# Performance work log

Measured on AMD Instinct MI355X. Metric: run time of the kernel, lower is better.

Reference implementation:

```python
import jax, jax.numpy as jnp
import numpy as np

NUM_HEADS = 16


def setup_inputs() -> dict:
    key = jax.random.key(0)
    k1, k2, k3 = jax.random.split(key, 3)
    B, S, E = 2, 2048, 1024
    hidden_states = jax.random.normal(k1, (B, S, E), dtype=jnp.float32)
    c_attn_w = jax.random.normal(k2, (E, 3 * E), dtype=jnp.float32) * 0.02
    c_attn_b = jnp.zeros((3 * E,), dtype=jnp.float32)
    c_proj_w = jax.random.normal(k3, (E, E), dtype=jnp.float32) * 0.02
    c_proj_b = jnp.zeros((E,), dtype=jnp.float32)
    return {
        "hidden_states": hidden_states,
        "c_attn_w": c_attn_w,
        "c_attn_b": c_attn_b,
        "c_proj_w": c_proj_w,
        "c_proj_b": c_proj_b,
    }


def reference(hidden_states, c_attn_w, c_attn_b, c_proj_w, c_proj_b):
    B, S, E = hidden_states.shape
    H = NUM_HEADS
    D = E // H
    # Conv1D: qkv projection -> [B, S, 3E]
    qkv = jnp.einsum("bse,ef->bsf", hidden_states, c_attn_w) + c_attn_b
    q, k, v = jnp.split(qkv, 3, axis=-1)
    # split heads -> [B, H, S, D]
    def heads(x):
        return x.reshape(B, S, H, D).transpose(0, 2, 1, 3)
    q, k, v = heads(q), heads(k), heads(v)
    # scaled QK^T -> [B, H, S, S]
    scale = jnp.asarray(D, dtype=q.dtype) ** 0.5
    attn_weights = jnp.einsum("bhqd,bhkd->bhqk", q, k) / scale
    # causal mask (bias buffer): True on/below diagonal
    causal = jnp.tril(jnp.ones((S, S), dtype=bool))
    mask_value = jnp.finfo(attn_weights.dtype).min
    attn_weights = jnp.where(causal[None, None, :, :], attn_weights, mask_value)
    attn_weights = jax.nn.softmax(attn_weights, axis=-1)
    # attn @ V -> merge heads -> [B, S, E]
    attn_out = jnp.einsum("bhqk,bhkd->bhqd", attn_weights, v)
    attn_out = attn_out.transpose(0, 2, 1, 3).reshape(B, S, E)
    # output projection (Conv1D)
    out = jnp.einsum("bse,ef->bsf", attn_out, c_proj_w) + c_proj_b
    return out
```

## Files before the change

kernel.cpp:

```cpp
#include <hip/hip_runtime.h>
#include <stdint.h>

typedef __attribute__((ext_vector_type(8))) __bf16 bf16x8;
typedef __attribute__((ext_vector_type(4))) __bf16 bf16x4;
typedef __attribute__((ext_vector_type(4))) float f32x4;

#define MFMA16(a, b, c) __builtin_amdgcn_mfma_f32_16x16x32_bf16(a, b, c, 0, 0, 0)

__device__ __forceinline__ void async_ld16(const __bf16* g, __bf16* lds_base) {
    __builtin_amdgcn_global_load_lds(
        (const __attribute__((address_space(1))) void*)g,
        (__attribute__((address_space(3))) void*)lds_base, 16, 0, 0);
}

__global__ __launch_bounds__(256) void k_prep(
    const float* __restrict__ hs, const float* __restrict__ w1,
    const float* __restrict__ w2, __bf16* __restrict__ hsb,
    __bf16* __restrict__ w1t, __bf16* __restrict__ w2t) {
    __shared__ __bf16 tile[32][33];
    int bid = blockIdx.x, tid = threadIdx.x;
    if (bid < 4096) {
        int i = (bid * 256 + tid) * 4;
        float4 v = *(const float4*)(hs + i);
        bf16x4 o;
        o.x = (__bf16)v.x; o.y = (__bf16)v.y; o.z = (__bf16)v.z; o.w = (__bf16)v.w;
        *(bf16x4*)(hsb + i) = o;
        return;
    }
    const float* in; __bf16* out; int C, tb;
    if (bid < 7168) { in = w1; out = w1t; C = 3072; tb = bid - 4096; }
    else            { in = w2; out = w2t; C = 1024; tb = bid - 7168; }
    const int R = 1024;
    int ntc = C >> 5;
    int c0 = (tb % ntc) * 32, r0 = (tb / ntc) * 32;
    int tx = tid & 31, ty = tid >> 5;
#pragma unroll
    for (int i = 0; i < 4; i++)
        tile[ty + i * 8][tx] = (__bf16)in[(size_t)(r0 + ty + i * 8) * C + c0 + tx];
    __syncthreads();
#pragma unroll
    for (int i = 0; i < 4; i++)
        out[(size_t)(c0 + ty + i * 8) * R + r0 + tx] = tile[tx][ty + i * 8];
}

__global__ __launch_bounds__(256, 2) void k_gemm_qkv(
    const __bf16* __restrict__ A, const __bf16* __restrict__ Bt,
    const float* __restrict__ bias,
    __bf16* __restrict__ Qo, __bf16* __restrict__ Ko, __bf16* __restrict__ Vo) {
    __shared__ __bf16 As[128 * 32];
    __shared__ __bf16 Bs[128 * 32];
    const int Kd = 1024;
    int n0 = blockIdx.x * 128, m0 = blockIdx.y * 128;
    int tid = threadIdx.x;
    int wv = tid >> 6, lane = tid & 63;
    int wm = (wv >> 1) * 64, wn = (wv & 1) * 64;
    int quad = lane >> 4, l16 = lane & 15;
    int lrow = lane >> 2, lcol = (lane & 3) * 8;
    f32x4 acc[4][4] = {};
    for (int k0 = 0; k0 < Kd; k0 += 32) {
        __syncthreads();
#pragma unroll
        for (int r = 0; r < 2; r++) {
            int row = r * 64 + wv * 16;
            async_ld16(&A[(size_t)(m0 + row + lrow) * Kd + k0 + lcol], &As[row * 32]);
            async_ld16(&Bt[(size_t)(n0 + row + lrow) * Kd + k0 + lcol], &Bs[row * 32]);
        }
        __syncthreads();
        bf16x8 af[4], bfr[4];
#pragma unroll
        for (int i = 0; i < 4; i++)
            af[i] = *(const bf16x8*)(&As[(wm + i * 16 + l16) * 32 + quad * 8]);
#pragma unroll
        for (int j = 0; j < 4; j++)
            bfr[j] = *(const bf16x8*)(&Bs[(wn + j * 16 + l16) * 32 + quad * 8]);
#pragma unroll
        for (int i = 0; i < 4; i++)
#pragma unroll
            for (int j = 0; j < 4; j++)
                acc[i][j] = MFMA16(af[i], bfr[j], acc[i][j]);
    }
#pragma unroll
    for (int i = 0; i < 4; i++) {
#pragma unroll
        for (int j = 0; j < 4; j++) {
            int n = n0 + wn + j * 16 + l16;
            float bv = bias[n];
            int sec = n >> 10, nl = n & 1023;
            int h = nl >> 6, d = nl & 63;
            int mbase = m0 + wm + i * 16 + quad * 4;
            int bb = mbase >> 11, s = mbase & 2047;
            if (sec == 2) {
                bf16x4 v4;
#pragma unroll
                for (int r = 0; r < 4; r++) v4[r] = (__bf16)(acc[i][j][r] + bv);
                *(bf16x4*)(&Vo[((size_t)(bb * 16 + h) * 64 + d) * 2048 + s]) = v4;
            } else {
                __bf16* dst = sec == 0 ? Qo : Ko;
                float scl = (sec == 0) ? 0.1803368801f : 1.0f;
#pragma unroll
                for (int r = 0; r < 4; r++)
                    dst[((size_t)(bb * 16 + h) * 2048 + (s + r)) * 64 + d] =
                        (__bf16)((acc[i][j][r] + bv) * scl);
            }
        }
    }
}

__global__ __launch_bounds__(256, 2) void k_gemm_proj(
    const __bf16* __restrict__ A, const __bf16* __restrict__ Bt,
    const float* __restrict__ bias, float* __restrict__ out) {
    __shared__ __bf16 As[64 * 32];
    __shared__ __bf16 Bs[128 * 32];
    const int Kd = 1024;
    int n0 = blockIdx.x * 128, m0 = blockIdx.y * 64;
    int tid = threadIdx.x;
    int wv = tid >> 6, lane = tid & 63;
    int wm = (wv >> 1) * 32, wn = (wv & 1) * 64;
    int quad = lane >> 4, l16 = lane & 15;
    int lrow = lane >> 2, lcol = (lane & 3) * 8;
    f32x4 acc[2][4] = {};
    for (int k0 = 0; k0 < Kd; k0 += 32) {
        __syncthreads();
        async_ld16(&A[(size_t)(m0 + wv * 16 + lrow) * Kd + k0 + lcol], &As[(wv * 16) * 32]);
#pragma unroll
        for (int r = 0; r < 2; r++) {
            int row = r * 64 + wv * 16;
            async_ld16(&Bt[(size_t)(n0 + row + lrow) * Kd + k0 + lcol], &Bs[row * 32]);
        }
        __syncthreads();
        bf16x8 af[2], bfr[4];
#pragma unroll
        for (int i = 0; i < 2; i++)
            af[i] = *(const bf16x8*)(&As[(wm + i * 16 + l16) * 32 + quad * 8]);
#pragma unroll
        for (int j = 0; j < 4; j++)
            bfr[j] = *(const bf16x8*)(&Bs[(wn + j * 16 + l16) * 32 + quad * 8]);
#pragma unroll
        for (int i = 0; i < 2; i++)
#pragma unroll
            for (int j = 0; j < 4; j++)
                acc[i][j] = MFMA16(af[i], bfr[j], acc[i][j]);
    }
#pragma unroll
    for (int i = 0; i < 2; i++) {
#pragma unroll
        for (int j = 0; j < 4; j++) {
            int n = n0 + wn + j * 16 + l16;
            float bv = bias[n];
#pragma unroll
            for (int r = 0; r < 4; r++) {
                int m = m0 + wm + i * 16 + quad * 4 + r;
                out[(size_t)m * 1024 + n] = acc[i][j][r] + bv;
            }
        }
    }
}

__device__ const int ATT_ORDER[24] = {7, 8, 10, 12, 14, 16, 18, 20, 22, 23, 6, 21,
                                      5, 19, 4, 17, 3, 15, 2, 13, 1, 11, 0, 9};

__global__ __launch_bounds__(256, 4) void k_attn(
    const __bf16* __restrict__ Qg, const __bf16* __restrict__ Kg,
    const __bf16* __restrict__ Vtg, __bf16* __restrict__ Op, float* __restrict__ Lp) {
    __shared__ __bf16 Ks[64 * 72];
    __shared__ __bf16 Vt[64 * 72];
    __shared__ __bf16 Ps[128 * 72];
    int bh = blockIdx.x & 31;
    int slot = ATT_ORDER[blockIdx.x >> 5];
    int t, k0, k1;
    if (slot < 8) { t = slot; k0 = 0; k1 = 2 * t + 2; }
    else { int i2 = slot - 8; t = 8 + (i2 >> 1); k0 = (i2 & 1) * 16; k1 = min(k0 + 16, 2 * t + 2); }
    const __bf16* Qp = Qg + (size_t)bh * 2048 * 64;
    const __bf16* Kp = Kg + (size_t)bh * 2048 * 64;
    const __bf16* Vp = Vtg + (size_t)bh * 64 * 2048;
    int tid = threadIdx.x, wv = tid >> 6, lane = tid & 63;
    int quad = lane >> 4, l16 = lane & 15;

    bf16x8 qf[2][2];
#pragma unroll
    for (int qn = 0; qn < 2; qn++)
#pragma unroll
        for (int ks = 0; ks < 2; ks++)
            qf[qn][ks] = *(const bf16x8*)(
                &Qp[(size_t)(t * 128 + wv * 32 + qn * 16 + l16) * 64 + ks * 32 + quad * 8]);
    float l_th[2] = {0.f, 0.f};
    f32x4 acc_o[2][4] = {};

    for (int kt = k0; kt < k1; kt++) {
        __syncthreads();
#pragma unroll
        for (int it = 0; it < 2; it++) {
            int idx = tid * 2 + it;
            int row = idx >> 3, cc = (idx & 7) * 8;
            *(uint4*)(&Ks[row * 72 + cc]) =
                *(const uint4*)(&Kp[(size_t)(kt * 64 + row) * 64 + cc]);
            *(uint4*)(&Vt[row * 72 + cc]) =
                *(const uint4*)(&Vp[(size_t)row * 2048 + kt * 64 + cc]);
        }
        __syncthreads();
        f32x4 s[2][4] = {};
#pragma unroll
        for (int ks = 0; ks < 2; ks++) {
            bf16x8 kf[4];
#pragma unroll
            for (int i = 0; i < 4; i++)
                kf[i] = *(const bf16x8*)(&Ks[(i * 16 + l16) * 72 + ks * 32 + quad * 8]);
#pragma unroll
            for (int i = 0; i < 4; i++)
#pragma unroll
                for (int qn = 0; qn < 2; qn++)
                    s[qn][i] = MFMA16(kf[i], qf[qn][ks], s[qn][i]);
        }
#pragma unroll
        for (int qn = 0; qn < 2; qn++) {
            int qmin = t * 128 + wv * 32 + qn * 16;
            if (kt * 64 + 63 > qmin) {
#pragma unroll
                for (int i = 0; i < 4; i++)
#pragma unroll
                    for (int r = 0; r < 4; r++)
                        if (kt * 64 + i * 16 + quad * 4 + r > qmin + l16) s[qn][i][r] = -1e30f;
            }
        }
#pragma unroll
        for (int qn = 0; qn < 2; qn++)
#pragma unroll
            for (int i = 0; i < 4; i++) {
                bf16x4 pk;
#pragma unroll
                for (int r = 0; r < 4; r++) {
                    float p = exp2f(s[qn][i][r]);
                    l_th[qn] += p;
                    pk[r] = (__bf16)p;
                }
                *(bf16x4*)(&Ps[(wv * 32 + qn * 16 + l16) * 72 + i * 16 + quad * 4]) = pk;
            }
#pragma unroll
        for (int ks = 0; ks < 2; ks++) {
            bf16x8 pf[2];
#pragma unroll
            for (int qn = 0; qn < 2; qn++)
                pf[qn] = *(const bf16x8*)(
                    &Ps[(wv * 32 + qn * 16 + l16) * 72 + ks * 32 + quad * 8]);
            bf16x8 vf[4];
#pragma unroll
            for (int i = 0; i < 4; i++)
                vf[i] = *(const bf16x8*)(&Vt[(i * 16 + l16) * 72 + ks * 32 + quad * 8]);
#pragma unroll
            for (int i = 0; i < 4; i++)
#pragma unroll
                for (int qn = 0; qn < 2; qn++)
                    acc_o[qn][i] = MFMA16(vf[i], pf[qn], acc_o[qn][i]);
        }
    }
    size_t pbase = (size_t)slot * 32 + bh;
#pragma unroll
    for (int qn = 0; qn < 2; qn++) {
        float ls = l_th[qn];
        ls += __shfl_xor(ls, 16);
        ls += __shfl_xor(ls, 32);
        int ql = wv * 32 + qn * 16 + l16;
        if (quad == 0) Lp[pbase * 128 + ql] = ls;
#pragma unroll
        for (int i = 0; i < 4; i++) {
            bf16x4 o4;
#pragma unroll
            for (int r = 0; r < 4; r++) o4[r] = (__bf16)acc_o[qn][i][r];
            *(bf16x4*)(&Op[(pbase * 128 + ql) * 64 + i * 16 + quad * 4]) = o4;
        }
    }
}

__global__ __launch_bounds__(256) void k_attn_combine(
    const __bf16* __restrict__ Op, const float* __restrict__ Lp,
    __bf16* __restrict__ AOb) {
    int gid = blockIdx.x * 256 + threadIdx.x;
    int d4 = gid & 15;
    int q = (gid >> 4) & 2047;
    int bh = gid >> 15;
    int t = q >> 7, ql = q & 127;
    int n = (t <= 7) ? 1 : 2;
    int base = (t <= 7) ? t : 8 + 2 * (t - 8);
    float L = 0.f, o[4] = {};
    for (int c = 0; c < n; c++) {
        size_t idx = (size_t)(base + c) * 32 + bh;
        L += Lp[idx * 128 + ql];
        bf16x4 p4 = *(const bf16x4*)(&Op[(idx * 128 + ql) * 64 + d4 * 4]);
#pragma unroll
        for (int r = 0; r < 4; r++) o[r] += (float)p4[r];
    }
    float inv = 1.f / L;
    int b = bh >> 4, h = bh & 15;
    bf16x4 o4;
#pragma unroll
    for (int r = 0; r < 4; r++) o4[r] = (__bf16)(o[r] * inv);
    *(bf16x4*)(&AOb[((size_t)b * 2048 + q) * 1024 + h * 64 + d4 * 4]) = o4;
}

extern "C" void kernel_launch(void* const* d_in, const int* in_sizes, int n_in,
                              void* d_out, int out_size, void* d_ws, size_t ws_size,
                              hipStream_t stream) {
    const float* hs = (const float*)d_in[0];
    const float* w1 = (const float*)d_in[1];
    const float* b1 = (const float*)d_in[2];
    const float* w2 = (const float*)d_in[3];
    const float* b2 = (const float*)d_in[4];
    float* out = (float*)d_out;

    char* ws = (char*)d_ws;
    __bf16* hsb = (__bf16*)(ws);
    __bf16* w1t = (__bf16*)(ws + (size_t)8 * 1024 * 1024);
    __bf16* w2t = (__bf16*)(ws + (size_t)14 * 1024 * 1024);
    __bf16* Qb  = (__bf16*)(ws + (size_t)16 * 1024 * 1024);
    __bf16* Kb  = (__bf16*)(ws + (size_t)24 * 1024 * 1024);
    __bf16* Vb  = (__bf16*)(ws + (size_t)32 * 1024 * 1024);
    __bf16* AOb = (__bf16*)(ws + (size_t)40 * 1024 * 1024);
    __bf16* Opart = (__bf16*)(ws);
    float*  Lpart = (float*)(ws + (size_t)13 * 1024 * 1024);

    k_prep<<<8192, 256, 0, stream>>>(hs, w1, w2, hsb, w1t, w2t);
    k_gemm_qkv<<<dim3(24, 32), 256, 0, stream>>>(hsb, w1t, b1, Qb, Kb, Vb);
    k_attn<<<768, 256, 0, stream>>>(Qb, Kb, Vb, Opart, Lpart);
    k_attn_combine<<<4096, 256, 0, stream>>>(Opart, Lpart, AOb);
    k_gemm_proj<<<dim3(8, 64), 256, 0, stream>>>(AOb, w2t, b2, out);
}
```

Before: 185.6 us.

## Double-buffer K/V tiles with async global-to-LDS loads and XOR swizzle

Replaces the synchronous register-staged K and V tile loads in the attention kernel with `global_load_lds` async copies into two LDS buffers. The next tile is prefetched while the current one is being computed, and a single barrier per iteration replaces the previous two. The padded 72-stride layout becomes an unpadded 64-stride layout with an XOR chunk swizzle to avoid LDS bank conflicts. Launch bounds drop from 4 to 3 blocks per CU, which cuts occupancy in exchange for the added LDS and overlap.

```diff
diff --git a/kernel.cpp b/kernel.cpp
--- a/kernel.cpp
+++ b/kernel.cpp
@@ -159,11 +159,11 @@
 __device__ const int ATT_ORDER[24] = {7, 8, 10, 12, 14, 16, 18, 20, 22, 23, 6, 21,
                                       5, 19, 4, 17, 3, 15, 2, 13, 1, 11, 0, 9};
 
-__global__ __launch_bounds__(256, 4) void k_attn(
+__global__ __launch_bounds__(256, 3) void k_attn(
     const __bf16* __restrict__ Qg, const __bf16* __restrict__ Kg,
     const __bf16* __restrict__ Vtg, __bf16* __restrict__ Op, float* __restrict__ Lp) {
-    __shared__ __bf16 Ks[64 * 72];
-    __shared__ __bf16 Vt[64 * 72];
+    __shared__ __bf16 Ksb[2][64 * 64];
+    __shared__ __bf16 Vtb[2][64 * 64];
     __shared__ __bf16 Ps[128 * 72];
     int bh = blockIdx.x & 31;
     int slot = ATT_ORDER[blockIdx.x >> 5];
@@ -175,6 +175,9 @@
     const __bf16* Vp = Vtg + (size_t)bh * 64 * 2048;
     int tid = threadIdx.x, wv = tid >> 6, lane = tid & 63;
     int quad = lane >> 4, l16 = lane & 15;
+    int rl = lane >> 3, sj = lane & 7;
+    int sgo = (sj ^ rl) << 3;
+    int swl = l16 & 7;
 
     bf16x8 qf[2][2];
 #pragma unroll
@@ -186,25 +189,31 @@
     float l_th[2] = {0.f, 0.f};
     f32x4 acc_o[2][4] = {};
 
+    auto stage = [&](int buf, int kt) {
+#pragma unroll
+        for (int half = 0; half < 2; half++) {
+            int r0 = wv * 16 + half * 8;
+            async_ld16(&Kp[(size_t)(kt * 64 + r0 + rl) * 64 + sgo], &Ksb[buf][r0 * 64]);
+            async_ld16(&Vp[(size_t)(r0 + rl) * 2048 + kt * 64 + sgo], &Vtb[buf][r0 * 64]);
+        }
+    };
+
+    stage(0, k0);
+    __syncthreads();
+
     for (int kt = k0; kt < k1; kt++) {
-        __syncthreads();
-#pragma unroll
-        for (int it = 0; it < 2; it++) {
-            int idx = tid * 2 + it;
-            int row = idx >> 3, cc = (idx & 7) * 8;
-            *(uint4*)(&Ks[row * 72 + cc]) =
-                *(const uint4*)(&Kp[(size_t)(kt * 64 + row) * 64 + cc]);
-            *(uint4*)(&Vt[row * 72 + cc]) =
-                *(const uint4*)(&Vp[(size_t)row * 2048 + kt * 64 + cc]);
-        }
-        __syncthreads();
+        int cur = (kt - k0) & 1;
+        if (kt + 1 < k1) stage(cur ^ 1, kt + 1);
+        const __bf16* Kc = Ksb[cur];
+        const __bf16* Vc = Vtb[cur];
         f32x4 s[2][4] = {};
 #pragma unroll
         for (int ks = 0; ks < 2; ks++) {
             bf16x8 kf[4];
 #pragma unroll
             for (int i = 0; i < 4; i++)
-                kf[i] = *(const bf16x8*)(&Ks[(i * 16 + l16) * 72 + ks * 32 + quad * 8]);
+                kf[i] = *(const bf16x8*)(
+                    &Kc[(i * 16 + l16) * 64 + (((ks * 4 + quad) ^ swl) << 3)]);
 #pragma unroll
             for (int i = 0; i < 4; i++)
 #pragma unroll
@@ -245,13 +254,15 @@
             bf16x8 vf[4];
 #pragma unroll
             for (int i = 0; i < 4; i++)
-                vf[i] = *(const bf16x8*)(&Vt[(i * 16 + l16) * 72 + ks * 32 + quad * 8]);
+                vf[i] = *(const bf16x8*)(
+                    &Vc[(i * 16 + l16) * 64 + (((ks * 4 + quad) ^ swl) << 3)]);
 #pragma unroll
             for (int i = 0; i < 4; i++)
 #pragma unroll
                 for (int qn = 0; qn < 2; qn++)
                     acc_o[qn][i] = MFMA16(vf[i], pf[qn], acc_o[qn][i]);
         }
+        __syncthreads();
     }
     size_t pbase = (size_t)slot * 32 + bh;
 #pragma unroll
```

After: 184.0 us. Within noise of the previous version (-0.8%).
